# Kernel tuning notes

Hardware: AMD Instinct MI355X
Metric: run time of the kernel (lower is better)

## Reference

```python
import jax, jax.numpy as jnp
import numpy as np

H, W, C = 80, 80, 64
R = 1.0  # rbf bandwidth (init kwarg r)


def setup_inputs() -> dict:
    key = jax.random.key(0)
    X = jax.random.normal(key, (H, W, C), dtype=jnp.float32)
    return {"X": X}


def reference(X):
    Hh, Ww, Cc = X.shape
    N = Hh * Ww

    # ---- coordinate similarity Ad (vectorized form of the O(N^2) loop) ----
    gr, gc = jnp.meshgrid(jnp.arange(Hh, dtype=X.dtype),
                          jnp.arange(Ww, dtype=X.dtype), indexing='ij')
    rf = gr.reshape(N)  # row coordinate i // W
    cf = gc.reshape(N)  # col coordinate i % W
    # squared euclidean distance between pixel coordinates, [N, N]
    d2 = (rf[:, None] - rf[None, :]) ** 2 + (cf[:, None] - cf[None, :]) ** 2
    Ad = jnp.exp(-d2 / (2.0 * R * R))
    # the python loop only fills i != j, so the diagonal stays 0
    Ad = Ad * (1.0 - jnp.eye(N, dtype=Ad.dtype))
    Ad = Ad / jnp.sum(Ad, axis=-1, keepdims=True)

    # ---- feature similarity As ----
    nodes = X.reshape(N, Cc)                      # [N, C]
    As = jax.nn.softmax(nodes @ nodes.T, axis=-1)  # [N, N], row softmax
    avg = jnp.mean(As, axis=-1, keepdims=True)     # per-row mean
    As = jnp.where(As < avg, jnp.zeros((), As.dtype), As)
    return Ad, As
```

## Files before the change

kernel.cpp:

```cpp
#include <hip/hip_runtime.h>

#define HH 80
#define NN 6400
#define CC 64
#define THR (1.0f / 6400.0f)

typedef _Float16 f16x8 __attribute__((ext_vector_type(8)));
typedef float float4v __attribute__((ext_vector_type(4)));

__global__ __launch_bounds__(256) void prep_kernel(
    const float* __restrict__ X,
    _Float16* __restrict__ Xhi, _Float16* __restrict__ Xlo,
    float* __restrict__ norms, float* __restrict__ denom,
    int* __restrict__ nmax, float* __restrict__ Stab)
{
    const int id = blockIdx.x * 256 + threadIdx.x;
    const float x = X[id];
    const _Float16 h = (_Float16)x;
    const float lo = x - (float)h;
    Xhi[id] = h;
    Xlo[id] = (_Float16)lo;

    float s = x * x;
#pragma unroll
    for (int m = 1; m < 64; m <<= 1) s += __shfl_xor(s, m, 64);
    const int lane = threadIdx.x & 63;
    if (lane == 0) {
        const int row = id >> 6;
        norms[row] = s;
        atomicMax(nmax, __float_as_int(s));
    }
    if (id < NN) denom[id] = 0.f;

    const int t = (int)threadIdx.x;
    if (blockIdx.x == 0 && t < HH) {
        float acc = 0.f;
        for (int k = 0; k < HH; k++) {
            const float d = (float)(t - k);
            acc += __expf(-0.5f * d * d);
        }
        Stab[t] = acc;
    }
}

__global__ __launch_bounds__(256) void pass1_kernel(
    const _Float16* __restrict__ Xhi, const _Float16* __restrict__ Xlo,
    const float* __restrict__ norms, const int* __restrict__ nmaxp,
    float* __restrict__ denom)
{
    const int tid = threadIdx.x;
    const int wave = tid >> 6, lane = tid & 63;
    const int q = lane >> 4, n16 = lane & 15;
    const int i0 = blockIdx.x * 256 + wave * 64;
    const int j0 = blockIdx.y * 256;
    const float nmax = __int_as_float(*nmaxp);

    f16x8 Ah[4][2], Al[4][2];
#pragma unroll
    for (int rt = 0; rt < 4; rt++) {
        const int row = i0 + rt * 16 + n16;
#pragma unroll
        for (int c = 0; c < 2; c++) {
            const int off = row * CC + c * 32 + q * 8;
            Ah[rt][c] = *(const f16x8*)(Xhi + off);
            Al[rt][c] = *(const f16x8*)(Xlo + off);
        }
    }
    float mh[4][4];
#pragma unroll
    for (int rt = 0; rt < 4; rt++)
#pragma unroll
        for (int r = 0; r < 4; r++)
            mh[rt][r] = sqrtf(norms[i0 + rt * 16 + q * 4 + r] * nmax);

    float cs[4][4];
#pragma unroll
    for (int rt = 0; rt < 4; rt++)
#pragma unroll
        for (int r = 0; r < 4; r++) cs[rt][r] = 0.f;

    for (int ct = 0; ct < 16; ct++) {
        const int col = j0 + ct * 16 + n16;
        f16x8 Bh[2], Bl[2];
#pragma unroll
        for (int c = 0; c < 2; c++) {
            const int off = col * CC + c * 32 + q * 8;
            Bh[c] = *(const f16x8*)(Xhi + off);
            Bl[c] = *(const f16x8*)(Xlo + off);
        }
#pragma unroll
        for (int rt = 0; rt < 4; rt++) {
            float4v acc = {0.f, 0.f, 0.f, 0.f};
#pragma unroll
            for (int c = 0; c < 2; c++) {
                acc = __builtin_amdgcn_mfma_f32_16x16x32_f16(Al[rt][c], Bh[c], acc, 0, 0, 0);
                acc = __builtin_amdgcn_mfma_f32_16x16x32_f16(Ah[rt][c], Bl[c], acc, 0, 0, 0);
                acc = __builtin_amdgcn_mfma_f32_16x16x32_f16(Ah[rt][c], Bh[c], acc, 0, 0, 0);
            }
#pragma unroll
            for (int r = 0; r < 4; r++)
                cs[rt][r] += __expf(acc[r] - mh[rt][r]);
        }
    }
#pragma unroll
    for (int rt = 0; rt < 4; rt++)
#pragma unroll
        for (int r = 0; r < 4; r++) {
            float v = cs[rt][r];
            v += __shfl_xor(v, 1, 64);
            v += __shfl_xor(v, 2, 64);
            v += __shfl_xor(v, 4, 64);
            v += __shfl_xor(v, 8, 64);
            if (n16 == 0)
                atomicAdd(&denom[i0 + rt * 16 + q * 4 + r], v);
        }
}

__global__ __launch_bounds__(256) void as_kernel(
    const _Float16* __restrict__ Xhi, const _Float16* __restrict__ Xlo,
    const float* __restrict__ norms, const int* __restrict__ nmaxp,
    const float* __restrict__ denom, float* __restrict__ As)
{
    __shared__ float sMh[256], sRden[256];
    const int tid = threadIdx.x;
    const int i0 = blockIdx.x * 256;
    const int j0 = blockIdx.y * 256;
    {
        const int i = i0 + tid;
        const float nmax = __int_as_float(*nmaxp);
        sMh[tid] = sqrtf(norms[i] * nmax);
        sRden[tid] = 1.0f / denom[i];
    }
    __syncthreads();

    const int wave = tid >> 6, lane = tid & 63;
    const int q = lane >> 4, n16 = lane & 15;
    const int iw = i0 + wave * 64;

    f16x8 Bh[4][2], Bl[4][2];
#pragma unroll
    for (int rt = 0; rt < 4; rt++) {
        const int row = iw + rt * 16 + n16;
#pragma unroll
        for (int c = 0; c < 2; c++) {
            const int off = row * CC + c * 32 + q * 8;
            Bh[rt][c] = *(const f16x8*)(Xhi + off);
            Bl[rt][c] = *(const f16x8*)(Xlo + off);
        }
    }
    float mh[4], rd[4];
#pragma unroll
    for (int rt = 0; rt < 4; rt++) {
        const int il = wave * 64 + rt * 16 + n16;
        mh[rt] = sMh[il];
        rd[rt] = sRden[il];
    }

    for (int ct = 0; ct < 16; ct++) {
        const int jt = j0 + ct * 16;
        f16x8 Ahh[2], All[2];
#pragma unroll
        for (int c = 0; c < 2; c++) {
            const int off = (jt + n16) * CC + c * 32 + q * 8;
            Ahh[c] = *(const f16x8*)(Xhi + off);
            All[c] = *(const f16x8*)(Xlo + off);
        }
        float4v acc[4];
#pragma unroll
        for (int rt = 0; rt < 4; rt++) acc[rt] = (float4v){0.f, 0.f, 0.f, 0.f};
#pragma unroll
        for (int rt = 0; rt < 4; rt++) {
#pragma unroll
            for (int c = 0; c < 2; c++) {
                acc[rt] = __builtin_amdgcn_mfma_f32_16x16x32_f16(All[c], Bh[rt][c], acc[rt], 0, 0, 0);
                acc[rt] = __builtin_amdgcn_mfma_f32_16x16x32_f16(Ahh[c], Bl[rt][c], acc[rt], 0, 0, 0);
                acc[rt] = __builtin_amdgcn_mfma_f32_16x16x32_f16(Ahh[c], Bh[rt][c], acc[rt], 0, 0, 0);
            }
        }
#pragma unroll
        for (int rt = 0; rt < 4; rt++) {
            float4v v;
#pragma unroll
            for (int r = 0; r < 4; r++) {
                const float e = __expf(acc[rt][r] - mh[rt]) * rd[rt];
                v[r] = (e < THR) ? 0.f : e;
            }
            *(float4v*)(As + (size_t)(iw + rt * 16 + n16) * NN + jt + q * 4) = v;
        }
    }
}

__global__ __launch_bounds__(256) void ad_kernel(
    const float* __restrict__ Stab, float* __restrict__ Ad)
{
    const int idx = blockIdx.x * 256 + threadIdx.x;
    const int i = idx / 1600;
    const int jq = (idx - i * 1600) * 4;
    const int ri = i / HH, ci = i - ri * HH;
    const int rj = jq / HH, cj0 = jq - rj * HH;
    const float rec = 1.0f / (Stab[ri] * Stab[ci] - 1.0f);
    const int dr = ri - rj;
    const float dr2 = (float)(dr * dr);
    float4v v;
#pragma unroll
    for (int r = 0; r < 4; r++) {
        const int dc = ci - (cj0 + r);
        const float d2 = dr2 + (float)(dc * dc);
        float ad = __expf(-0.5f * d2) * rec;
        if (i == jq + r) ad = 0.f;
        v[r] = ad;
    }
    *(float4v*)(Ad + (size_t)idx * 4) = v;
}

extern "C" void kernel_launch(void* const* d_in, const int* in_sizes, int n_in,
                              void* d_out, int out_size, void* d_ws, size_t ws_size,
                              hipStream_t stream) {
    const float* X = (const float*)d_in[0];
    float* Ad = (float*)d_out;
    float* As = Ad + (size_t)NN * NN;

    char* w = (char*)d_ws;
    _Float16* Xhi = (_Float16*)(w);
    _Float16* Xlo = (_Float16*)(w + 819200);
    float* norms  = (float*)(w + 1638400);
    float* denom  = (float*)(w + 1664000);
    int*   nmax   = (int*)(w + 1689600);
    float* Stab   = (float*)(w + 1689664);

    prep_kernel<<<dim3((NN * CC) / 256), dim3(256), 0, stream>>>(
        X, Xhi, Xlo, norms, denom, nmax, Stab);
    pass1_kernel<<<dim3(25, 25), dim3(256), 0, stream>>>(
        Xhi, Xlo, norms, nmax, denom);
    as_kernel<<<dim3(25, 25), dim3(256), 0, stream>>>(
        Xhi, Xlo, norms, nmax, denom, As);
    ad_kernel<<<dim3(NN * NN / 4 / 256), dim3(256), 0, stream>>>(Stab, Ad);
}
```

Before: 466.2 us.

## Fuse Ad generation into As tile kernel and skip far-row exponentials

Removes the separate Ad kernel and writes each 256x256 Ad tile from the same blocks that write As, using per-tile shared-memory tables of pixel row/column coordinates and per-row normalisation reciprocals. Rows whose pixel-row distance to the tile is large, and elements with squared distance above a cutoff, are written as zero without computing exp, since they would underflow anyway. This saves a kernel launch and most of the exp work for Ad, but lengthens each tile block, which now also streams a second 256x256 output.

```diff
diff --git a/kernel.cpp b/kernel.cpp
--- a/kernel.cpp
+++ b/kernel.cpp
@@ -116,12 +116,14 @@
         }
 }
 
-__global__ __launch_bounds__(256) void as_kernel(
+__global__ __launch_bounds__(256) void tile_kernel(
     const _Float16* __restrict__ Xhi, const _Float16* __restrict__ Xlo,
     const float* __restrict__ norms, const int* __restrict__ nmaxp,
-    const float* __restrict__ denom, float* __restrict__ As)
+    const float* __restrict__ denom, const float* __restrict__ Stab,
+    float* __restrict__ As, float* __restrict__ Ad)
 {
-    __shared__ float sMh[256], sRden[256];
+    __shared__ float sMh[256], sRden[256], sRec[256];
+    __shared__ int sRI[256], sCJ[256];
     const int tid = threadIdx.x;
     const int i0 = blockIdx.x * 256;
     const int j0 = blockIdx.y * 256;
@@ -130,6 +132,12 @@
         const float nmax = __int_as_float(*nmaxp);
         sMh[tid] = sqrtf(norms[i] * nmax);
         sRden[tid] = 1.0f / denom[i];
+        const int ri = i / HH, ci = i - ri * HH;
+        sRec[tid] = 1.0f / (Stab[ri] * Stab[ci] - 1.0f);
+        sRI[tid] = (ri << 8) | ci;
+        const int j = j0 + tid;
+        const int rj = j / HH, cj = j - rj * HH;
+        sCJ[tid] = (rj << 8) | cj;
     }
     __syncthreads();
 
@@ -188,29 +196,34 @@
             *(float4v*)(As + (size_t)(iw + rt * 16 + n16) * NN + jt + q * 4) = v;
         }
     }
-}
-
-__global__ __launch_bounds__(256) void ad_kernel(
-    const float* __restrict__ Stab, float* __restrict__ Ad)
-{
-    const int idx = blockIdx.x * 256 + threadIdx.x;
-    const int i = idx / 1600;
-    const int jq = (idx - i * 1600) * 4;
-    const int ri = i / HH, ci = i - ri * HH;
-    const int rj = jq / HH, cj0 = jq - rj * HH;
-    const float rec = 1.0f / (Stab[ri] * Stab[ci] - 1.0f);
-    const int dr = ri - rj;
-    const float dr2 = (float)(dr * dr);
-    float4v v;
-#pragma unroll
-    for (int r = 0; r < 4; r++) {
-        const int dc = ci - (cj0 + r);
-        const float d2 = dr2 + (float)(dc * dc);
-        float ad = __expf(-0.5f * d2) * rec;
-        if (i == jq + r) ad = 0.f;
-        v[r] = ad;
-    }
-    *(float4v*)(Ad + (size_t)idx * 4) = v;
+
+    const int rjlo = j0 / HH, rjhi = (j0 + 255) / HH;
+    for (int it = 0; it < 64; it++) {
+        const int il = it * 4 + wave;
+        const int i = i0 + il;
+        const int rc = sRI[il];
+        const int ri = rc >> 8, ci = rc & 255;
+        const int mind = (ri < rjlo) ? (rjlo - ri) : (ri > rjhi ? ri - rjhi : 0);
+        float4v v;
+        if (mind >= 14) {
+            v = (float4v){0.f, 0.f, 0.f, 0.f};
+        } else {
+            const float rec = sRec[il];
+#pragma unroll
+            for (int r = 0; r < 4; r++) {
+                const int jl = lane * 4 + r;
+                const int jc = sCJ[jl];
+                const int rj = jc >> 8, cj = jc & 255;
+                const int dr = ri - rj, dc = ci - cj;
+                const int d2 = dr * dr + dc * dc;
+                float ad = (d2 == 0 && i == j0 + jl) ? 0.f
+                         : (d2 > 180) ? 0.f
+                         : __expf(-0.5f * (float)d2) * rec;
+                v[r] = ad;
+            }
+        }
+        *(float4v*)(Ad + (size_t)i * NN + j0 + lane * 4) = v;
+    }
 }
 
 extern "C" void kernel_launch(void* const* d_in, const int* in_sizes, int n_in,
@@ -232,7 +245,6 @@
         X, Xhi, Xlo, norms, denom, nmax, Stab);
     pass1_kernel<<<dim3(25, 25), dim3(256), 0, stream>>>(
         Xhi, Xlo, norms, nmax, denom);
-    as_kernel<<<dim3(25, 25), dim3(256), 0, stream>>>(
-        Xhi, Xlo, norms, nmax, denom, As);
-    ad_kernel<<<dim3(NN * NN / 4 / 256), dim3(256), 0, stream>>>(Stab, Ad);
-}
+    tile_kernel<<<dim3(25, 25), dim3(256), 0, stream>>>(
+        Xhi, Xlo, norms, nmax, denom, Stab, As, Ad);
+}
```

New measurement: 497.2 us. +6.7%, slower.
